# Kernel optimization log

Hardware: AMD Instinct MI355X
Metric: run time of the kernel (lower is better)

Reference implementation:

```python
import jax, jax.numpy as jnp
import numpy as np

# ---- config constants (mirror UniformViewTransformer init) ----
GRID = (128, 128, 8)              # (X, Y, Z)
PC_RANGE = (-51.2, -51.2, -3.0, 51.2, 51.2, 5.0)
VOXEL = (0.8, 0.8, 1.0)
NUM_CAMS = 6
STRIDE = 16
IMG_H, IMG_W = 256, 704
C_FEAT = 64
HF, WF = IMG_H // STRIDE, IMG_W // STRIDE  # 16, 44


def _voxel_grid():
    xs = jnp.linspace(PC_RANGE[0] + VOXEL[0] / 2, PC_RANGE[3] - VOXEL[0] / 2, GRID[0])
    ys = jnp.linspace(PC_RANGE[1] + VOXEL[1] / 2, PC_RANGE[4] - VOXEL[1] / 2, GRID[1])
    zs = jnp.linspace(PC_RANGE[2] + VOXEL[2] / 2, PC_RANGE[5] - VOXEL[2] / 2, GRID[2])
    zz, yy, xx = jnp.meshgrid(zs, ys, xs, indexing='ij')   # (Z,Y,X) each
    return jnp.stack([xx, yy, zz], axis=0).astype(jnp.float32)  # (3,Z,Y,X)


def setup_inputs() -> dict:
    key = jax.random.key(0)
    k1, k2, k3 = jax.random.split(key, 3)
    img_feats = jax.random.normal(k1, (NUM_CAMS, C_FEAT, HF, WF), dtype=jnp.float32)
    # realistic pinhole intrinsics (pixel-space projection)
    K = jnp.array([[400.0, 0.0, 352.0, 0.0],
                   [0.0, 400.0, 128.0, 0.0],
                   [0.0, 0.0, 1.0, 0.0],
                   [0.0, 0.0, 0.0, 1.0]], dtype=jnp.float32)
    cam2img = jnp.broadcast_to(K, (NUM_CAMS, 4, 4)).copy()
    # ego2cam: yaw rotation per camera + small perturbation + translation
    yaws = jnp.arange(NUM_CAMS, dtype=jnp.float32) * (2 * np.pi / NUM_CAMS)
    c, s = jnp.cos(yaws), jnp.sin(yaws)
    z = jnp.zeros_like(c); o = jnp.ones_like(c)
    R = jnp.stack([jnp.stack([c, -s, z, z], -1),
                   jnp.stack([s, c, z, z], -1),
                   jnp.stack([z, z, o, z], -1),
                   jnp.stack([z, z, z, o], -1)], axis=1)  # (N,4,4)
    ego2cam = R + 0.01 * jax.random.normal(k2, (NUM_CAMS, 4, 4), dtype=jnp.float32)
    ego2cam = ego2cam.at[:, 2, 3].add(2.0)  # push points in front of cameras
    return {
        'img_feats': img_feats,
        'ego2cam': ego2cam,
        'cam2img': cam2img,
        'voxel_coords': _voxel_grid(),
    }


def _grid_sample_points(feat, u_norm, v_norm):
    """Bilinear grid_sample, align_corners=True, padding_mode='zeros'.
    feat: (BN,C,Hf,Wf); u_norm,v_norm: (BN,P) in [-1,1]. Returns (BN,C,P)."""
    BN, C, Hf, Wf = feat.shape
    x = (u_norm + 1.0) * 0.5 * (Wf - 1)
    y = (v_norm + 1.0) * 0.5 * (Hf - 1)
    x0 = jnp.floor(x); y0 = jnp.floor(y)
    wx1 = x - x0; wx0 = 1.0 - wx1
    wy1 = y - y0; wy0 = 1.0 - wy1
    x0i = x0.astype(jnp.int32); x1i = x0i + 1
    y0i = y0.astype(jnp.int32); y1i = y0i + 1

    def corner(xi, yi, w):
        m = ((xi >= 0) & (xi < Wf) & (yi >= 0) & (yi < Hf)).astype(feat.dtype)
        xc = jnp.clip(xi, 0, Wf - 1)
        yc = jnp.clip(yi, 0, Hf - 1)
        g = jax.vmap(lambda f, yy, xx: f[:, yy, xx])(feat, yc, xc)  # (BN,C,P)
        return g * (w * m)[:, None, :]

    return (corner(x0i, y0i, wx0 * wy0) + corner(x1i, y0i, wx1 * wy0)
            + corner(x0i, y1i, wx0 * wy1) + corner(x1i, y1i, wx1 * wy1))


def reference(img_feats, ego2cam, cam2img, voxel_coords):
    BN, C, Hf, Wf = img_feats.shape
    _, Z, Y, X = voxel_coords.shape
    P = Z * Y * X
    pts = voxel_coords.reshape(3, P)                       # (3,P)
    pts_h = jnp.concatenate([pts, jnp.ones((1, P), pts.dtype)], axis=0)  # (4,P)
    proj = jnp.einsum('nij,njk->nik', cam2img, ego2cam)    # (BN,4,4)
    img_pts = jnp.einsum('nik,kp->nip', proj, pts_h)       # (BN,4,P)
    depth = img_pts[:, 2, :]
    eps = 1e-6
    u = img_pts[:, 0, :] / (depth + eps)
    v = img_pts[:, 1, :] / (depth + eps)
    valid = (depth > 0.1) & (u >= 0) & (u <= IMG_W - 1) & (v >= 0) & (v <= IMG_H - 1)
    uf = u / float(STRIDE)
    vf = v / float(STRIDE)
    u_norm = 2.0 * (uf / max(Wf - 1, 1)) - 1.0
    v_norm = 2.0 * (vf / max(Hf - 1, 1)) - 1.0
    u_norm = jnp.where(valid, u_norm, 2.0)
    v_norm = jnp.where(valid, v_norm, 2.0)

    sampled = _grid_sample_points(img_feats, u_norm, v_norm)  # (BN,C,P)

    B = BN // NUM_CAMS
    sampled = sampled.reshape(B, NUM_CAMS, C, P)
    vmask = valid.reshape(B, NUM_CAMS, 1, P).astype(sampled.dtype)
    denom = jnp.clip(vmask.sum(axis=1), 1.0, None)          # (B,1,P)
    fused = sampled.sum(axis=1) / denom                     # mean fusion
    return fused.reshape(B, C, Z, Y, X)
```

## Files before the change

kernel.cpp:

```cpp
#include <hip/hip_runtime.h>
#include <hip/hip_fp16.h>

#define NUM_CAMS 6
#define C_FEAT   64
#define HF       16
#define WF       44
#define NPTS     (128*128*8)
#define FEAT_ELEMS (NUM_CAMS*C_FEAT*HF*WF)
#define PPB      64
#define NTHREADS 512

__global__ __launch_bounds__(256) void uvt_prep(const float* __restrict__ in,
                                                const float* __restrict__ ego2cam,
                                                const float* __restrict__ cam2img,
                                                __half* __restrict__ featsT,
                                                float* __restrict__ projws) {
    const int blk = blockIdx.x;
    if (blk < NUM_CAMS * HF) {
        __shared__ float s[WF][C_FEAT + 1];
        const int n = blk / HF, y = blk % HF;
        const float* src = in + n * C_FEAT * HF * WF + y * WF;
        for (int e = threadIdx.x; e < C_FEAT * WF; e += 256) {
            const int c = e / WF, x = e - c * WF;
            s[x][c] = src[c * HF * WF + x];
        }
        __syncthreads();
        __half* dst = featsT + (n * HF + y) * WF * C_FEAT;
        for (int e = threadIdx.x; e < C_FEAT * WF; e += 256) {
            const int x = e >> 6, c = e & 63;
            dst[e] = __float2half(s[x][c]);
        }
    } else {
        const int t = threadIdx.x;
        if (t < NUM_CAMS * 12) {
            const int cam = t / 12, e = t - cam * 12;
            const int i = e >> 2, j = e & 3;
            const float* A = cam2img + cam * 16;
            const float* B = ego2cam + cam * 16;
            float sum = 0.f;
            #pragma unroll
            for (int k = 0; k < 4; ++k) sum += A[i*4 + k] * B[k*4 + j];
            projws[cam * 12 + e] = sum;
        }
    }
}

struct alignas(32) PC {
    __half2 w00, w10, w01, w11;
    int base, dx, dy, valid;
};

__global__ __launch_bounds__(NTHREADS) void uvt_fuse(
    const __half* __restrict__ featsT,
    const float* __restrict__ projws,
    const float* __restrict__ vox,
    float* __restrict__ out)
{
    __shared__ PC    s_pc[NUM_CAMS][PPB];
    __shared__ float s_out[PPB][C_FEAT + 1];

    const int tid = threadIdx.x;
    const int p0  = blockIdx.x * PPB;

    if (tid < NUM_CAMS * PPB) {
        const int cam = __builtin_amdgcn_readfirstlane(tid >> 6);
        const int lp  = tid & 63;
        const int p   = p0 + lp;
        const float* M = projws + cam * 12;

        const float px = vox[p];
        const float py = vox[NPTS + p];
        const float pz = vox[2 * NPTS + p];
        const float ud = M[0]*px + M[1]*py + M[2]*pz  + M[3];
        const float vd = M[4]*px + M[5]*py + M[6]*pz  + M[7];
        const float d  = M[8]*px + M[9]*py + M[10]*pz + M[11];
        const float id = 1.0f / (d + 1e-6f);
        const float u  = ud * id;
        const float v  = vd * id;
        const bool valid = (d > 0.1f) && (u >= 0.f) && (u <= 703.f)
                                      && (v >= 0.f) && (v <= 255.f);
        PC pc;
        if (valid) {
            const float x  = u * 0.0625f;
            const float y  = v * 0.0625f;
            const float xf = floorf(x), yf = floorf(y);
            const int   x0 = (int)xf,   y0 = (int)yf;
            const float wx1 = x - xf,  wy1 = y - yf;
            const float wx0 = 1.f - wx1, wy0 = 1.f - wy1;
            const bool bx = (x0 < WF - 1);
            const bool by = (y0 < HF - 1);
            pc.w00 = __float2half2_rn(wx0 * wy0);
            pc.w10 = __float2half2_rn(bx ? wx1 * wy0 : 0.f);
            pc.w01 = __float2half2_rn(by ? wx0 * wy1 : 0.f);
            pc.w11 = __float2half2_rn((bx && by) ? wx1 * wy1 : 0.f);
            pc.base = ((cam * HF + y0) * WF + x0) << 6;
            pc.dx   = bx ? C_FEAT : 0;
            pc.dy   = by ? WF * C_FEAT : 0;
            pc.valid = 1;
        } else {
            pc.w00 = pc.w10 = pc.w01 = pc.w11 = __float2half2_rn(0.f);
            pc.base = pc.dx = pc.dy = 0;
            pc.valid = 0;
        }
        s_pc[cam][lp] = pc;
    }
    __syncthreads();

    const int oct = tid & 7;
    const int pl  = tid >> 3;
    int vm = 0, cnt = 0;
    #pragma unroll
    for (int cam = 0; cam < NUM_CAMS; ++cam) {
        const int v = s_pc[cam][pl].valid;
        vm |= v << cam;
        cnt += v;
    }
    const float inv = 1.0f / (float)(cnt > 0 ? cnt : 1);

    float2 a0 = {0.f,0.f}, a1 = {0.f,0.f}, a2 = {0.f,0.f}, a3 = {0.f,0.f};
    #pragma unroll
    for (int cam = 0; cam < NUM_CAMS; ++cam) {
        if ((vm >> cam) & 1) {
            const PC pc = s_pc[cam][pl];
            const __half* b = featsT + pc.base + (oct << 3);
            const uint4 r00 = *(const uint4*)(b);
            const uint4 r10 = *(const uint4*)(b + pc.dx);
            const uint4 r01 = *(const uint4*)(b + pc.dy);
            const uint4 r11 = *(const uint4*)(b + pc.dx + pc.dy);

            #define BC(u_) __builtin_bit_cast(__half2, u_)
            __half2 s0 = __hmul2(pc.w00, BC(r00.x));
            s0 = __hfma2(pc.w10, BC(r10.x), s0);
            s0 = __hfma2(pc.w01, BC(r01.x), s0);
            s0 = __hfma2(pc.w11, BC(r11.x), s0);
            __half2 s1 = __hmul2(pc.w00, BC(r00.y));
            s1 = __hfma2(pc.w10, BC(r10.y), s1);
            s1 = __hfma2(pc.w01, BC(r01.y), s1);
            s1 = __hfma2(pc.w11, BC(r11.y), s1);
            __half2 s2 = __hmul2(pc.w00, BC(r00.z));
            s2 = __hfma2(pc.w10, BC(r10.z), s2);
            s2 = __hfma2(pc.w01, BC(r01.z), s2);
            s2 = __hfma2(pc.w11, BC(r11.z), s2);
            __half2 s3 = __hmul2(pc.w00, BC(r00.w));
            s3 = __hfma2(pc.w10, BC(r10.w), s3);
            s3 = __hfma2(pc.w01, BC(r01.w), s3);
            s3 = __hfma2(pc.w11, BC(r11.w), s3);
            #undef BC

            const float2 f0 = __half22float2(s0);
            const float2 f1 = __half22float2(s1);
            const float2 f2 = __half22float2(s2);
            const float2 f3 = __half22float2(s3);
            a0.x += f0.x; a0.y += f0.y;
            a1.x += f1.x; a1.y += f1.y;
            a2.x += f2.x; a2.y += f2.y;
            a3.x += f3.x; a3.y += f3.y;
        }
    }

    const int cb = oct << 3;
    s_out[pl][cb + 0] = a0.x * inv;
    s_out[pl][cb + 1] = a0.y * inv;
    s_out[pl][cb + 2] = a1.x * inv;
    s_out[pl][cb + 3] = a1.y * inv;
    s_out[pl][cb + 4] = a2.x * inv;
    s_out[pl][cb + 5] = a2.y * inv;
    s_out[pl][cb + 6] = a3.x * inv;
    s_out[pl][cb + 7] = a3.y * inv;
    __syncthreads();

    #pragma unroll
    for (int i = 0; i < 8; ++i) {
        const int idx = tid + NTHREADS * i;
        const int c   = idx >> 6;
        const int lp  = idx & 63;
        out[c * NPTS + p0 + lp] = s_out[lp][c];
    }
}

extern "C" void kernel_launch(void* const* d_in, const int* in_sizes, int n_in,
                              void* d_out, int out_size, void* d_ws, size_t ws_size,
                              hipStream_t stream) {
    const float* img_feats = (const float*)d_in[0];
    const float* ego2cam   = (const float*)d_in[1];
    const float* cam2img   = (const float*)d_in[2];
    const float* vox       = (const float*)d_in[3];
    float* out = (float*)d_out;

    __half* featsT = (__half*)d_ws;
    float*  projws = (float*)((char*)d_ws + FEAT_ELEMS * sizeof(__half));

    uvt_prep<<<NUM_CAMS * HF + 1, 256, 0, stream>>>(img_feats, ego2cam, cam2img,
                                                    featsT, projws);
    uvt_fuse<<<NPTS / PPB, NTHREADS, 0, stream>>>(featsT, projws, vox, out);
}
```

Measured before the change: 20.77 us.

## Shrink per-point sample record, alias LDS buffers, and flatten feature transpose

The per-camera sample record shrinks from 32 to 16 bytes by packing the four half weights into two half2 values and the dx/dy/valid fields into one flags word. The record array and the output staging tile now share one LDS buffer, which needs an extra barrier before the output tile is written. Together these cut LDS footprint per block, aiming for more resident blocks, and halve LDS reads of the sample records. The prep kernel's transpose switches from an LDS-staged per-row version to a direct one-element-per-thread gather over many more blocks, which trades coalesced reads for more parallelism.

```diff
diff --git a/kernel.cpp b/kernel.cpp
--- a/kernel.cpp
+++ b/kernel.cpp
@@ -16,20 +16,15 @@
                                                 __half* __restrict__ featsT,
                                                 float* __restrict__ projws) {
     const int blk = blockIdx.x;
-    if (blk < NUM_CAMS * HF) {
-        __shared__ float s[WF][C_FEAT + 1];
-        const int n = blk / HF, y = blk % HF;
-        const float* src = in + n * C_FEAT * HF * WF + y * WF;
-        for (int e = threadIdx.x; e < C_FEAT * WF; e += 256) {
-            const int c = e / WF, x = e - c * WF;
-            s[x][c] = src[c * HF * WF + x];
-        }
-        __syncthreads();
-        __half* dst = featsT + (n * HF + y) * WF * C_FEAT;
-        for (int e = threadIdx.x; e < C_FEAT * WF; e += 256) {
-            const int x = e >> 6, c = e & 63;
-            dst[e] = __float2half(s[x][c]);
-        }
+    if (blk < FEAT_ELEMS / 256) {
+        const int g   = blk * 256 + threadIdx.x;
+        const int c   = g & 63;
+        const int pix = g >> 6;
+        const int x   = pix % WF;
+        const int t2  = pix / WF;
+        const int y   = t2 % HF;
+        const int n   = t2 / HF;
+        featsT[g] = __float2half(in[((n * C_FEAT + c) * HF + y) * WF + x]);
     } else {
         const int t = threadIdx.x;
         if (t < NUM_CAMS * 12) {
@@ -45,9 +40,11 @@
     }
 }
 
-struct alignas(32) PC {
-    __half2 w00, w10, w01, w11;
-    int base, dx, dy, valid;
+struct alignas(16) PCP {
+    __half2  wA;
+    __half2  wB;
+    int      base;
+    unsigned flags;
 };
 
 __global__ __launch_bounds__(NTHREADS) void uvt_fuse(
@@ -56,8 +53,9 @@
     const float* __restrict__ vox,
     float* __restrict__ out)
 {
-    __shared__ PC    s_pc[NUM_CAMS][PPB];
-    __shared__ float s_out[PPB][C_FEAT + 1];
+    __shared__ __align__(16) char ldsbuf[PPB * (C_FEAT + 1) * sizeof(float)];
+    PCP   (*s_pc)[PPB]         = (PCP (*)[PPB])ldsbuf;
+    float (*s_out)[C_FEAT + 1] = (float (*)[C_FEAT + 1])ldsbuf;
 
     const int tid = threadIdx.x;
     const int p0  = blockIdx.x * PPB;
@@ -79,7 +77,7 @@
         const float v  = vd * id;
         const bool valid = (d > 0.1f) && (u >= 0.f) && (u <= 703.f)
                                       && (v >= 0.f) && (v <= 255.f);
-        PC pc;
+        PCP pc;
         if (valid) {
             const float x  = u * 0.0625f;
             const float y  = v * 0.0625f;
@@ -89,18 +87,17 @@
             const float wx0 = 1.f - wx1, wy0 = 1.f - wy1;
             const bool bx = (x0 < WF - 1);
             const bool by = (y0 < HF - 1);
-            pc.w00 = __float2half2_rn(wx0 * wy0);
-            pc.w10 = __float2half2_rn(bx ? wx1 * wy0 : 0.f);
-            pc.w01 = __float2half2_rn(by ? wx0 * wy1 : 0.f);
-            pc.w11 = __float2half2_rn((bx && by) ? wx1 * wy1 : 0.f);
-            pc.base = ((cam * HF + y0) * WF + x0) << 6;
-            pc.dx   = bx ? C_FEAT : 0;
-            pc.dy   = by ? WF * C_FEAT : 0;
-            pc.valid = 1;
+            pc.wA = __halves2half2(__float2half(wx0 * wy0),
+                                   __float2half(bx ? wx1 * wy0 : 0.f));
+            pc.wB = __halves2half2(__float2half(by ? wx0 * wy1 : 0.f),
+                                   __float2half((bx && by) ? wx1 * wy1 : 0.f));
+            pc.base  = ((cam * HF + y0) * WF + x0) << 6;
+            pc.flags = (bx ? 64u : 0u)
+                     | ((by ? (unsigned)(WF * C_FEAT) : 0u) << 16)
+                     | 0x80000000u;
         } else {
-            pc.w00 = pc.w10 = pc.w01 = pc.w11 = __float2half2_rn(0.f);
-            pc.base = pc.dx = pc.dy = 0;
-            pc.valid = 0;
+            pc.wA = pc.wB = __halves2half2(__float2half(0.f), __float2half(0.f));
+            pc.base = 0; pc.flags = 0u;
         }
         s_pc[cam][lp] = pc;
     }
@@ -108,43 +105,44 @@
 
     const int oct = tid & 7;
     const int pl  = tid >> 3;
-    int vm = 0, cnt = 0;
+    float2 a0 = {0.f,0.f}, a1 = {0.f,0.f}, a2 = {0.f,0.f}, a3 = {0.f,0.f};
+    int cnt = 0;
+
     #pragma unroll
     for (int cam = 0; cam < NUM_CAMS; ++cam) {
-        const int v = s_pc[cam][pl].valid;
-        vm |= v << cam;
-        cnt += v;
-    }
-    const float inv = 1.0f / (float)(cnt > 0 ? cnt : 1);
-
-    float2 a0 = {0.f,0.f}, a1 = {0.f,0.f}, a2 = {0.f,0.f}, a3 = {0.f,0.f};
-    #pragma unroll
-    for (int cam = 0; cam < NUM_CAMS; ++cam) {
-        if ((vm >> cam) & 1) {
-            const PC pc = s_pc[cam][pl];
+        const PCP pc = s_pc[cam][pl];
+        const unsigned fl = pc.flags;
+        cnt += (int)(fl >> 31);
+        if (fl >> 31) {
+            const int dx = (int)(fl & 0xFFFFu);
+            const int dy = (int)((fl >> 16) & 0x7FFFu);
             const __half* b = featsT + pc.base + (oct << 3);
             const uint4 r00 = *(const uint4*)(b);
-            const uint4 r10 = *(const uint4*)(b + pc.dx);
-            const uint4 r01 = *(const uint4*)(b + pc.dy);
-            const uint4 r11 = *(const uint4*)(b + pc.dx + pc.dy);
+            const uint4 r10 = *(const uint4*)(b + dx);
+            const uint4 r01 = *(const uint4*)(b + dy);
+            const uint4 r11 = *(const uint4*)(b + dx + dy);
 
+            const __half2 w00 = __low2half2(pc.wA);
+            const __half2 w10 = __high2half2(pc.wA);
+            const __half2 w01 = __low2half2(pc.wB);
+            const __half2 w11 = __high2half2(pc.wB);
             #define BC(u_) __builtin_bit_cast(__half2, u_)
-            __half2 s0 = __hmul2(pc.w00, BC(r00.x));
-            s0 = __hfma2(pc.w10, BC(r10.x), s0);
-            s0 = __hfma2(pc.w01, BC(r01.x), s0);
-            s0 = __hfma2(pc.w11, BC(r11.x), s0);
-            __half2 s1 = __hmul2(pc.w00, BC(r00.y));
-            s1 = __hfma2(pc.w10, BC(r10.y), s1);
-            s1 = __hfma2(pc.w01, BC(r01.y), s1);
-            s1 = __hfma2(pc.w11, BC(r11.y), s1);
-            __half2 s2 = __hmul2(pc.w00, BC(r00.z));
-            s2 = __hfma2(pc.w10, BC(r10.z), s2);
-            s2 = __hfma2(pc.w01, BC(r01.z), s2);
-            s2 = __hfma2(pc.w11, BC(r11.z), s2);
-            __half2 s3 = __hmul2(pc.w00, BC(r00.w));
-            s3 = __hfma2(pc.w10, BC(r10.w), s3);
-            s3 = __hfma2(pc.w01, BC(r01.w), s3);
-            s3 = __hfma2(pc.w11, BC(r11.w), s3);
+            __half2 s0 = __hmul2(w00, BC(r00.x));
+            s0 = __hfma2(w10, BC(r10.x), s0);
+            s0 = __hfma2(w01, BC(r01.x), s0);
+            s0 = __hfma2(w11, BC(r11.x), s0);
+            __half2 s1 = __hmul2(w00, BC(r00.y));
+            s1 = __hfma2(w10, BC(r10.y), s1);
+            s1 = __hfma2(w01, BC(r01.y), s1);
+            s1 = __hfma2(w11, BC(r11.y), s1);
+            __half2 s2 = __hmul2(w00, BC(r00.z));
+            s2 = __hfma2(w10, BC(r10.z), s2);
+            s2 = __hfma2(w01, BC(r01.z), s2);
+            s2 = __hfma2(w11, BC(r11.z), s2);
+            __half2 s3 = __hmul2(w00, BC(r00.w));
+            s3 = __hfma2(w10, BC(r10.w), s3);
+            s3 = __hfma2(w01, BC(r01.w), s3);
+            s3 = __hfma2(w11, BC(r11.w), s3);
             #undef BC
 
             const float2 f0 = __half22float2(s0);
@@ -157,7 +155,9 @@
             a3.x += f3.x; a3.y += f3.y;
         }
     }
+    __syncthreads();
 
+    const float inv = 1.0f / (float)(cnt > 0 ? cnt : 1);
     const int cb = oct << 3;
     s_out[pl][cb + 0] = a0.x * inv;
     s_out[pl][cb + 1] = a0.y * inv;
@@ -190,7 +190,7 @@
     __half* featsT = (__half*)d_ws;
     float*  projws = (float*)((char*)d_ws + FEAT_ELEMS * sizeof(__half));
 
-    uvt_prep<<<NUM_CAMS * HF + 1, 256, 0, stream>>>(img_feats, ego2cam, cam2img,
-                                                    featsT, projws);
+    uvt_prep<<<FEAT_ELEMS / 256 + 1, 256, 0, stream>>>(img_feats, ego2cam, cam2img,
+                                                       featsT, projws);
     uvt_fuse<<<NPTS / PPB, NTHREADS, 0, stream>>>(featsT, projws, vox, out);
 }
```

New measurement: 19.96 us. -3.9%, faster.
